# Performance work log

Measured on AMD Instinct MI355X. Metric: run time of the kernel, lower is better.

The kernel has to match this reference:

```python
import jax, jax.numpy as jnp
import numpy as np

N, D_IN, R, D_OUT, U = 500000, 128, 256, 64, 10000
EPS = 1e-8


def _vb_layer(m, v, W_mu, W_lv, relu_out):
    # Variational Bayes linear layer, moment propagation:
    #   out_mean = m @ W_mu
    #   out_var  = v @ (W_mu^2 + W_var) + m^2 @ W_var,  W_var = exp(W_lv)
    W_var = jnp.exp(W_lv)
    M = m @ W_mu
    V = v @ (W_mu * W_mu + W_var) + (m * m) @ W_var
    if relu_out:
        gate = (M > 0).astype(M.dtype)
        M = M * gate
        V = V * gate
    return M, V


def setup_inputs() -> dict:
    key = jax.random.key(0)
    ks = jax.random.split(key, 6)
    X = jax.random.normal(ks[0], (N, D_IN), jnp.float32)
    X_idx = jnp.sort(jax.random.randint(ks[1], (N,), 0, U, dtype=jnp.int32))
    W_mu0 = jax.random.normal(ks[2], (D_IN, R), jnp.float32) / np.sqrt(D_IN)
    W_lv0 = jax.random.normal(ks[3], (D_IN, R), jnp.float32) * 0.1 - 4.0
    W_mu1 = jax.random.normal(ks[4], (R, D_OUT), jnp.float32) / np.sqrt(R)
    W_lv1 = jax.random.normal(ks[5], (R, D_OUT), jnp.float32) * 0.1 - 4.0
    return {"X": X, "X_idx": X_idx, "W_mu0": W_mu0, "W_lv0": W_lv0,
            "W_mu1": W_mu1, "W_lv1": W_lv1}


def reference(X, X_idx, W_mu0, W_lv0, W_mu1, W_lv1):
    m, v = _vb_layer(X, jnp.zeros_like(X), W_mu0, W_lv0, True)   # [N, R]
    m, v = _vb_layer(m, v, W_mu1, W_lv1, False)                  # [N, D_OUT]
    v = jnp.maximum(v, EPS)
    inv_v = 1.0 / v
    # precision-weighted aggregation per group id (replaces per-uid loop)
    var_inv_sum = jax.ops.segment_sum(inv_v, X_idx, num_segments=U) + EPS
    mean_sum = jax.ops.segment_sum(m * inv_v, X_idx, num_segments=U)
    emb_var = 1.0 / var_inv_sum          # [U, D_OUT]
    emb_mean = mean_sum * emb_var        # [U, D_OUT]
    return emb_mean, emb_var
```

## Files before the change

kernel.cpp:

```cpp
#include <hip/hip_runtime.h>
#include <stdint.h>

#define N_ROWS 500000
#define U_DIM 10000
#define EPSV 1e-8f
#define NT16 31250

typedef __attribute__((ext_vector_type(8))) short bf16x8;
typedef __attribute__((ext_vector_type(4))) float f32x4;

__device__ __forceinline__ short f2bf(float f) {
  unsigned u = __float_as_uint(f);
  u += 0x7fffu + ((u >> 16) & 1u);
  return (short)(u >> 16);
}

__global__ void prep_weights(const float* __restrict__ Wmu0,
                             const float* __restrict__ Wlv0,
                             const float* __restrict__ Wmu1,
                             const float* __restrict__ Wlv1,
                             short* __restrict__ wgt) {
  int i = blockIdx.x * blockDim.x + threadIdx.x;
  if (i < 32768) {
    int c = i & 255, k = i >> 8;
    int rc = c >> 5, ct = (c >> 4) & 1, n = c & 15;
    int kt = k >> 5, q = (k >> 3) & 3, u = k & 7;
    int lane = q * 16 + n;
    float mu = Wmu0[k * 256 + c];
    float ev = __expf(Wlv0[k * 256 + c]);
    wgt[((((rc * 2 + 0) * 2 + ct) * 4 + kt) * 64 + lane) * 8 + u] = f2bf(mu);
    wgt[((((rc * 2 + 1) * 2 + ct) * 4 + kt) * 64 + lane) * 8 + u] = f2bf(ev);
  } else if (i < 49152) {
    int i2 = i - 32768;
    int o = i2 & 63, j = i2 >> 6;
    int rc = j >> 5, jl = j & 31;
    int q = (jl >> 2) & 3;
    int u = ((jl >> 4) << 2) | (jl & 3);
    int ct1 = o >> 4, n = o & 15;
    int lane = q * 16 + n;
    float mu = Wmu1[j * 64 + o];
    float ev = __expf(Wlv1[j * 64 + o]);
    int b = 65536 + (((rc * 4 + ct1) * 3 + 0) * 64 + lane) * 8 + u;
    wgt[b]        = f2bf(mu);
    wgt[b + 512]  = f2bf(mu * mu + ev);
    wgt[b + 1024] = f2bf(ev);
  }
}

__global__ __launch_bounds__(256, 4) void vb_fused(
    const float* __restrict__ X, const int* __restrict__ Xidx,
    const short* __restrict__ wgt, float* __restrict__ out) {
  __shared__ __align__(16) short stage[2][8192];

  const int tid  = threadIdx.x;
  const int w    = tid >> 6;
  const int lane = tid & 63;
  const int n    = lane & 15;
  const int q    = lane >> 4;
  const int T    = blockIdx.x * 4 + w;
  const bool active = (T < NT16);
  const int row0 = active ? T * 16 : (N_ROWS - 16);

  const f32x4 zf4 = {0.f, 0.f, 0.f, 0.f};
  const int lane8 = lane * 8;

  bf16x8 a_m[4], a_sq[4];
  {
    const float* xr = X + (size_t)(row0 + n) * 128;
#pragma unroll
    for (int kt = 0; kt < 4; ++kt) {
      float xf[8];
      *(float4*)&xf[0] = *(const float4*)&xr[kt * 32 + q * 8];
      *(float4*)&xf[4] = *(const float4*)&xr[kt * 32 + q * 8 + 4];
#pragma unroll
      for (int u = 0; u < 8; ++u) {
        a_m[kt][u]  = f2bf(xf[u]);
        a_sq[kt][u] = f2bf(xf[u] * xf[u]);
      }
    }
  }

  f32x4 accm1[4], accv1[4];
#pragma unroll
  for (int c = 0; c < 4; ++c) { accm1[c] = zf4; accv1[c] = zf4; }

  const char* gbase = (const char*)wgt;
#define ISSUE_STAGE(rc_, buf_)                                                 \
  do {                                                                         \
    _Pragma("unroll")                                                          \
    for (int s_ = 0; s_ < 4; ++s_) {                                           \
      __builtin_amdgcn_global_load_lds(                                        \
          (const __attribute__((address_space(1))) unsigned int*)              \
              (gbase + (rc_) * 16384 + s_ * 4096 + tid * 16),                  \
          (__attribute__((address_space(3))) unsigned int*)                    \
              ((char*)&stage[buf_][0] + s_ * 4096 + (w << 10)),                \
          16, 0, 0);                                                           \
    }                                                                          \
  } while (0)

  ISSUE_STAGE(0, 0);

#pragma unroll
  for (int rc = 0; rc < 8; ++rc) {
    __syncthreads();
    if (rc < 7) ISSUE_STAGE(rc + 1, (rc + 1) & 1);

    const short* st = &stage[rc & 1][0];

    f32x4 accm0[2], accv0[2];
    accm0[0] = zf4; accm0[1] = zf4; accv0[0] = zf4; accv0[1] = zf4;
#pragma unroll
    for (int kt = 0; kt < 4; ++kt) {
#pragma unroll
      for (int ct = 0; ct < 2; ++ct) {
        bf16x8 bm = *(const bf16x8*)&st[((0 * 2 + ct) * 4 + kt) * 512 + lane8];
        bf16x8 bv = *(const bf16x8*)&st[((1 * 2 + ct) * 4 + kt) * 512 + lane8];
        accm0[ct] = __builtin_amdgcn_mfma_f32_16x16x32_bf16(bm, a_m[kt],  accm0[ct], 0, 0, 0);
        accv0[ct] = __builtin_amdgcn_mfma_f32_16x16x32_bf16(bv, a_sq[kt], accv0[ct], 0, 0, 0);
      }
    }

    bf16x8 am, av, asq;
#pragma unroll
    for (int u = 0; u < 8; ++u) {
      float m = accm0[u >> 2][u & 3];
      float v = accv0[u >> 2][u & 3];
      if (!(m > 0.f)) { m = 0.f; v = 0.f; }
      am[u]  = f2bf(m);
      av[u]  = f2bf(v);
      asq[u] = f2bf(m * m);
    }

    const short* l1b = wgt + 65536 + rc * 6144 + lane8;
#pragma unroll
    for (int ct1 = 0; ct1 < 4; ++ct1) {
      const short* fb = l1b + ct1 * 1536;
      bf16x8 b1 = *(const bf16x8*)&fb[0];
      bf16x8 b2 = *(const bf16x8*)&fb[512];
      bf16x8 b3 = *(const bf16x8*)&fb[1024];
      accm1[ct1] = __builtin_amdgcn_mfma_f32_16x16x32_bf16(am,  b1, accm1[ct1], 0, 0, 0);
      accv1[ct1] = __builtin_amdgcn_mfma_f32_16x16x32_bf16(av,  b2, accv1[ct1], 0, 0, 0);
      accv1[ct1] = __builtin_amdgcn_mfma_f32_16x16x32_bf16(asq, b3, accv1[ct1], 0, 0, 0);
    }
  }
#undef ISSUE_STAGE

  if (!active) return;
  float* meanp = out;
  float* varp  = out + U_DIM * 64;
  int4 idx4 = *(const int4*)&Xidx[row0 + q * 4];
  int uid[4] = {idx4.x, idx4.y, idx4.z, idx4.w};
#pragma unroll
  for (int ct = 0; ct < 4; ++ct) {
    const int o = ct * 16 + n;
    float sm = 0.f, sv = 0.f;
    int cur = uid[0];
#pragma unroll
    for (int reg = 0; reg < 4; ++reg) {
      float v1 = fmaxf(accv1[ct][reg], EPSV);
      float inv = 1.0f / v1;
      float mi  = accm1[ct][reg] * inv;
      if (uid[reg] != cur) {
        atomicAdd(&meanp[cur * 64 + o], sm);
        atomicAdd(&varp[cur * 64 + o], sv);
        sm = 0.f; sv = 0.f; cur = uid[reg];
      }
      sm += mi; sv += inv;
    }
    atomicAdd(&meanp[cur * 64 + o], sm);
    atomicAdd(&varp[cur * 64 + o], sv);
  }
}

__global__ void finalize(float* __restrict__ out) {
  int i = blockIdx.x * blockDim.x + threadIdx.x;
  if (i < U_DIM * 64) {
    float s = out[U_DIM * 64 + i];
    float var = 1.0f / (s + EPSV);
    out[U_DIM * 64 + i] = var;
    out[i] = out[i] * var;
  }
}

extern "C" void kernel_launch(void* const* d_in, const int* in_sizes, int n_in,
                              void* d_out, int out_size, void* d_ws, size_t ws_size,
                              hipStream_t stream) {
  (void)in_sizes; (void)n_in; (void)out_size; (void)ws_size;
  const float* X    = (const float*)d_in[0];
  const int*   Xidx = (const int*)d_in[1];
  const float* Wmu0 = (const float*)d_in[2];
  const float* Wlv0 = (const float*)d_in[3];
  const float* Wmu1 = (const float*)d_in[4];
  const float* Wlv1 = (const float*)d_in[5];
  float* out = (float*)d_out;
  short* wgt = (short*)d_ws;

  hipMemsetAsync(d_out, 0, (size_t)U_DIM * 64 * 2 * sizeof(float), stream);
  prep_weights<<<192, 256, 0, stream>>>(Wmu0, Wlv0, Wmu1, Wlv1, wgt);
  vb_fused<<<7813, 256, 0, stream>>>(X, Xidx, wgt, out);
  finalize<<<(U_DIM * 64 + 255) / 256, 256, 0, stream>>>(out);
}
```

Before: 584.3 us.

## Process two 16-row tiles per wave to reuse staged weight fragments

Each wave now handles 32 rows (two 16-row MFMA tiles) instead of 16, so every weight fragment loaded from LDS or global is used for two tiles and the grid is halved. The squared-input fragments are recomputed per k-tile from the bf16 inputs instead of being held in registers, which saves register space. Launch bounds drop from 4 to 3 blocks per SM to leave room for the doubled accumulators. This lowers occupancy and raises per-wave register pressure.

```diff
diff --git a/kernel.cpp b/kernel.cpp
--- a/kernel.cpp
+++ b/kernel.cpp
@@ -4,7 +4,7 @@
 #define N_ROWS 500000
 #define U_DIM 10000
 #define EPSV 1e-8f
-#define NT16 31250
+#define NT32 15625
 
 typedef __attribute__((ext_vector_type(8))) short bf16x8;
 typedef __attribute__((ext_vector_type(4))) float f32x4;
@@ -13,6 +13,9 @@
   unsigned u = __float_as_uint(f);
   u += 0x7fffu + ((u >> 16) & 1u);
   return (short)(u >> 16);
+}
+__device__ __forceinline__ float bf2f(short s) {
+  return __uint_as_float(((unsigned)(unsigned short)s) << 16);
 }
 
 __global__ void prep_weights(const float* __restrict__ Wmu0,
@@ -47,7 +50,7 @@
   }
 }
 
-__global__ __launch_bounds__(256, 4) void vb_fused(
+__global__ __launch_bounds__(256, 3) void vb_fused(
     const float* __restrict__ X, const int* __restrict__ Xidx,
     const short* __restrict__ wgt, float* __restrict__ out) {
   __shared__ __align__(16) short stage[2][8192];
@@ -58,31 +61,33 @@
   const int n    = lane & 15;
   const int q    = lane >> 4;
   const int T    = blockIdx.x * 4 + w;
-  const bool active = (T < NT16);
-  const int row0 = active ? T * 16 : (N_ROWS - 16);
+  const bool active = (T < NT32);
+  const int row0 = active ? T * 32 : (N_ROWS - 32);
 
   const f32x4 zf4 = {0.f, 0.f, 0.f, 0.f};
   const int lane8 = lane * 8;
 
-  bf16x8 a_m[4], a_sq[4];
+  bf16x8 amA[4], amB[4];
   {
-    const float* xr = X + (size_t)(row0 + n) * 128;
+    const float* xa = X + (size_t)(row0 + n) * 128;
+    const float* xb = X + (size_t)(row0 + 16 + n) * 128;
 #pragma unroll
     for (int kt = 0; kt < 4; ++kt) {
       float xf[8];
-      *(float4*)&xf[0] = *(const float4*)&xr[kt * 32 + q * 8];
-      *(float4*)&xf[4] = *(const float4*)&xr[kt * 32 + q * 8 + 4];
-#pragma unroll
-      for (int u = 0; u < 8; ++u) {
-        a_m[kt][u]  = f2bf(xf[u]);
-        a_sq[kt][u] = f2bf(xf[u] * xf[u]);
-      }
-    }
-  }
-
-  f32x4 accm1[4], accv1[4];
-#pragma unroll
-  for (int c = 0; c < 4; ++c) { accm1[c] = zf4; accv1[c] = zf4; }
+      *(float4*)&xf[0] = *(const float4*)&xa[kt * 32 + q * 8];
+      *(float4*)&xf[4] = *(const float4*)&xa[kt * 32 + q * 8 + 4];
+#pragma unroll
+      for (int u = 0; u < 8; ++u) amA[kt][u] = f2bf(xf[u]);
+      *(float4*)&xf[0] = *(const float4*)&xb[kt * 32 + q * 8];
+      *(float4*)&xf[4] = *(const float4*)&xb[kt * 32 + q * 8 + 4];
+#pragma unroll
+      for (int u = 0; u < 8; ++u) amB[kt][u] = f2bf(xf[u]);
+    }
+  }
+
+  f32x4 cmA[4], cmB[4], cvA[4], cvB[4];
+#pragma unroll
+  for (int c = 0; c < 4; ++c) { cmA[c] = zf4; cmB[c] = zf4; cvA[c] = zf4; cvB[c] = zf4; }
 
   const char* gbase = (const char*)wgt;
 #define ISSUE_STAGE(rc_, buf_)                                                 \
@@ -107,28 +112,37 @@
 
     const short* st = &stage[rc & 1][0];
 
-    f32x4 accm0[2], accv0[2];
-    accm0[0] = zf4; accm0[1] = zf4; accv0[0] = zf4; accv0[1] = zf4;
+    f32x4 pmA[2], pmB[2], pvA[2], pvB[2];
+    pmA[0] = zf4; pmA[1] = zf4; pmB[0] = zf4; pmB[1] = zf4;
+    pvA[0] = zf4; pvA[1] = zf4; pvB[0] = zf4; pvB[1] = zf4;
 #pragma unroll
     for (int kt = 0; kt < 4; ++kt) {
+      bf16x8 sqA, sqB;
+#pragma unroll
+      for (int u = 0; u < 8; ++u) {
+        float fa = bf2f(amA[kt][u]); sqA[u] = f2bf(fa * fa);
+        float fb = bf2f(amB[kt][u]); sqB[u] = f2bf(fb * fb);
+      }
 #pragma unroll
       for (int ct = 0; ct < 2; ++ct) {
         bf16x8 bm = *(const bf16x8*)&st[((0 * 2 + ct) * 4 + kt) * 512 + lane8];
         bf16x8 bv = *(const bf16x8*)&st[((1 * 2 + ct) * 4 + kt) * 512 + lane8];
-        accm0[ct] = __builtin_amdgcn_mfma_f32_16x16x32_bf16(bm, a_m[kt],  accm0[ct], 0, 0, 0);
-        accv0[ct] = __builtin_amdgcn_mfma_f32_16x16x32_bf16(bv, a_sq[kt], accv0[ct], 0, 0, 0);
+        pmA[ct] = __builtin_amdgcn_mfma_f32_16x16x32_bf16(bm, amA[kt], pmA[ct], 0, 0, 0);
+        pmB[ct] = __builtin_amdgcn_mfma_f32_16x16x32_bf16(bm, amB[kt], pmB[ct], 0, 0, 0);
+        pvA[ct] = __builtin_amdgcn_mfma_f32_16x16x32_bf16(bv, sqA, pvA[ct], 0, 0, 0);
+        pvB[ct] = __builtin_amdgcn_mfma_f32_16x16x32_bf16(bv, sqB, pvB[ct], 0, 0, 0);
       }
     }
 
-    bf16x8 am, av, asq;
+    bf16x8 gmA, gvA, gqA, gmB, gvB, gqB;
 #pragma unroll
     for (int u = 0; u < 8; ++u) {
-      float m = accm0[u >> 2][u & 3];
-      float v = accv0[u >> 2][u & 3];
+      float m = pmA[u >> 2][u & 3], v = pvA[u >> 2][u & 3];
       if (!(m > 0.f)) { m = 0.f; v = 0.f; }
-      am[u]  = f2bf(m);
-      av[u]  = f2bf(v);
-      asq[u] = f2bf(m * m);
+      gmA[u] = f2bf(m); gvA[u] = f2bf(v); gqA[u] = f2bf(m * m);
+      m = pmB[u >> 2][u & 3]; v = pvB[u >> 2][u & 3];
+      if (!(m > 0.f)) { m = 0.f; v = 0.f; }
+      gmB[u] = f2bf(m); gvB[u] = f2bf(v); gqB[u] = f2bf(m * m);
     }
 
     const short* l1b = wgt + 65536 + rc * 6144 + lane8;
@@ -138,9 +152,12 @@
       bf16x8 b1 = *(const bf16x8*)&fb[0];
       bf16x8 b2 = *(const bf16x8*)&fb[512];
       bf16x8 b3 = *(const bf16x8*)&fb[1024];
-      accm1[ct1] = __builtin_amdgcn_mfma_f32_16x16x32_bf16(am,  b1, accm1[ct1], 0, 0, 0);
-      accv1[ct1] = __builtin_amdgcn_mfma_f32_16x16x32_bf16(av,  b2, accv1[ct1], 0, 0, 0);
-      accv1[ct1] = __builtin_amdgcn_mfma_f32_16x16x32_bf16(asq, b3, accv1[ct1], 0, 0, 0);
+      cmA[ct1] = __builtin_amdgcn_mfma_f32_16x16x32_bf16(gmA, b1, cmA[ct1], 0, 0, 0);
+      cmB[ct1] = __builtin_amdgcn_mfma_f32_16x16x32_bf16(gmB, b1, cmB[ct1], 0, 0, 0);
+      cvA[ct1] = __builtin_amdgcn_mfma_f32_16x16x32_bf16(gvA, b2, cvA[ct1], 0, 0, 0);
+      cvB[ct1] = __builtin_amdgcn_mfma_f32_16x16x32_bf16(gvB, b2, cvB[ct1], 0, 0, 0);
+      cvA[ct1] = __builtin_amdgcn_mfma_f32_16x16x32_bf16(gqA, b3, cvA[ct1], 0, 0, 0);
+      cvB[ct1] = __builtin_amdgcn_mfma_f32_16x16x32_bf16(gqB, b3, cvB[ct1], 0, 0, 0);
     }
   }
 #undef ISSUE_STAGE
@@ -148,28 +165,35 @@
   if (!active) return;
   float* meanp = out;
   float* varp  = out + U_DIM * 64;
-  int4 idx4 = *(const int4*)&Xidx[row0 + q * 4];
-  int uid[4] = {idx4.x, idx4.y, idx4.z, idx4.w};
-#pragma unroll
-  for (int ct = 0; ct < 4; ++ct) {
-    const int o = ct * 16 + n;
-    float sm = 0.f, sv = 0.f;
-    int cur = uid[0];
-#pragma unroll
-    for (int reg = 0; reg < 4; ++reg) {
-      float v1 = fmaxf(accv1[ct][reg], EPSV);
-      float inv = 1.0f / v1;
-      float mi  = accm1[ct][reg] * inv;
-      if (uid[reg] != cur) {
-        atomicAdd(&meanp[cur * 64 + o], sm);
-        atomicAdd(&varp[cur * 64 + o], sv);
-        sm = 0.f; sv = 0.f; cur = uid[reg];
-      }
-      sm += mi; sv += inv;
-    }
-    atomicAdd(&meanp[cur * 64 + o], sm);
-    atomicAdd(&varp[cur * 64 + o], sv);
-  }
+#define EPILOG(CM_, CV_, BASE_)                                                \
+  do {                                                                         \
+    int4 idx4 = *(const int4*)&Xidx[(BASE_) + q * 4];                          \
+    int uid[4] = {idx4.x, idx4.y, idx4.z, idx4.w};                             \
+    _Pragma("unroll")                                                          \
+    for (int ct = 0; ct < 4; ++ct) {                                           \
+      const int o = ct * 16 + n;                                               \
+      float sm = 0.f, sv = 0.f;                                                \
+      int cur = uid[0];                                                        \
+      _Pragma("unroll")                                                        \
+      for (int reg = 0; reg < 4; ++reg) {                                      \
+        float v1 = fmaxf(CV_[ct][reg], EPSV);                                  \
+        float inv = 1.0f / v1;                                                 \
+        float mi  = CM_[ct][reg] * inv;                                        \
+        if (uid[reg] != cur) {                                                 \
+          atomicAdd(&meanp[cur * 64 + o], sm);                                 \
+          atomicAdd(&varp[cur * 64 + o], sv);                                  \
+          sm = 0.f; sv = 0.f; cur = uid[reg];                                  \
+        }                                                                      \
+        sm += mi; sv += inv;                                                   \
+      }                                                                        \
+      atomicAdd(&meanp[cur * 64 + o], sm);                                     \
+      atomicAdd(&varp[cur * 64 + o], sv);                                      \
+    }                                                                          \
+  } while (0)
+
+  EPILOG(cmA, cvA, row0);
+  EPILOG(cmB, cvB, row0 + 16);
+#undef EPILOG
 }
 
 __global__ void finalize(float* __restrict__ out) {
@@ -197,6 +221,6 @@
 
   hipMemsetAsync(d_out, 0, (size_t)U_DIM * 64 * 2 * sizeof(float), stream);
   prep_weights<<<192, 256, 0, stream>>>(Wmu0, Wlv0, Wmu1, Wlv1, wgt);
-  vb_fused<<<7813, 256, 0, stream>>>(X, Xidx, wgt, out);
+  vb_fused<<<3907, 256, 0, stream>>>(X, Xidx, wgt, out);
   finalize<<<(U_DIM * 64 + 255) / 256, 256, 0, stream>>>(out);
 }
```

Measured after the change: 771.8 us. 1.32x slower.
